# Optimization experiments

Hardware: AMD Instinct MI355X
Metric: run time of the kernel (lower is better)

Reference implementation:

```python
import jax, jax.numpy as jnp
import numpy as np
import math

M = 0.2
S = 30.0
COS_M = math.cos(M); SIN_M = math.sin(M)
TH = math.cos(math.pi - M)          # threshold used in torch.where
MM = math.sin(math.pi - M) * M      # linear penalty past threshold
EPS_LS = 0.1                        # CrossEntropyLoss label_smoothing


def _normalize(a, axis=-1):
    return a / jnp.clip(jnp.linalg.norm(a, axis=axis, keepdims=True), 1e-12)


def setup_inputs() -> dict:
    key = jax.random.key(0)
    k1, k2, k3, k4, k5 = jax.random.split(key, 5)
    B, D, C = 2048, 512, 10000
    x = jax.random.normal(k1, (B, D), dtype=jnp.float32)
    label = jax.random.randint(k2, (B,), 0, 1000)  # valid class ids, ~2 per class
    std = math.sqrt(2.0 / (C + D))  # xavier_normal gain=1
    weight = jax.random.normal(k3, (C, D), dtype=jnp.float32) * std    # self.weight (w)
    weight_m = jax.random.normal(k4, (C, D), dtype=jnp.float32) * std  # self.weight_m (wq)
    weight_n = jax.random.uniform(k5, (C, D), dtype=jnp.float32)       # self.weight_n (wk)
    return {"x": x, "label": label, "weight": weight, "weight_m": weight_m, "weight_n": weight_n}


def reference(x, label, weight, weight_m, weight_n):
    B = x.shape[0]
    C = weight.shape[0]
    xn = _normalize(x)                                   # [B, D]

    # ---- AAM (ArcFace) branch ----
    cosine = xn @ _normalize(weight).T                   # [B, C]
    sine = jnp.sqrt(jnp.clip(1.0 - cosine * cosine, 0.0, 1.0))
    phi = cosine * COS_M - sine * SIN_M
    phi = jnp.where(cosine - TH > 0, phi, cosine - MM)
    one_hot = jax.nn.one_hot(label, C, dtype=cosine.dtype)
    output = (one_hot * phi + (1.0 - one_hot) * cosine) * S
    logp = jax.nn.log_softmax(output, axis=-1)
    q_target = one_hot * (1.0 - EPS_LS) + EPS_LS / C     # label smoothing
    aam_loss = -jnp.mean(jnp.sum(q_target * logp, axis=-1))

    # ---- Control-Contrastive branch ----
    label_matrix = label[:, None] == label[None, :]      # [B, B] bool
    q = xn @ _normalize(weight_m[label]).T               # [B, B]
    k = xn @ _normalize(weight_n[label]).T               # [B, B]
    sim = q * k                                          # elementwise, [B, B]

    lm = label_matrix.astype(sim.dtype)
    ap_m = jnp.sum(sim * lm, axis=1) / jnp.sum(lm, axis=1)  # masked row means, [B]
    ap = jnp.diagonal(sim)                                   # [B]
    an = jnp.where(label_matrix, 0.0, sim)                   # [B, B]

    cos_ap = jnp.clip(ap, 0.0, 1.0)
    sin_ap = jnp.sqrt(jnp.clip(1.0 - cos_ap, 0.0, 1.0))
    cos_apm = jnp.clip(ap_m, 0.0, 1.0)
    sin_apm = jnp.sqrt(jnp.clip(1.0 - cos_apm, 0.0, 1.0))
    cos_an = jnp.clip(an, 0.0, 1.0)
    sin_an = jnp.sqrt(jnp.clip(1.0 - cos_an, 0.0, 1.0))

    phi_pm_c = cos_ap * cos_apm - sin_ap * sin_apm       # [B]
    phi_pm_s = jnp.sqrt(jnp.clip(1.0 - phi_pm_c, 0.0, 1.0))
    phi_pm = phi_pm_c * COS_M - phi_pm_s * SIN_M
    logit_neg = 1.0 - phi_pm                              # [B]

    # torch broadcasting [B,B]*[B] -> broadcast over rows (axis 0)
    phi_nm_s = sin_an * cos_apm[None, :] + cos_an * sin_apm[None, :]
    phi_nm_c = jnp.sqrt(jnp.clip(1.0 - phi_nm_s, 0.0, 1.0))
    phi_nm = phi_nm_s * COS_M - phi_nm_c * SIN_M          # [B, B]

    # ragged boolean-indexed logsumexp == masked logsumexp over whole matrix
    lse_n = jax.nn.logsumexp(jnp.where(label_matrix, -jnp.inf, phi_nm))
    lse_neg = jax.nn.logsumexp(logit_neg)
    cc_loss = jax.nn.softplus(lse_n + lse_neg)

    return aam_loss + cc_loss
```

## Files before the change

### kernel.cpp

```cpp
#include <hip/hip_runtime.h>
#include <hip/hip_bf16.h>

typedef unsigned short u16;
typedef unsigned char u8;
typedef unsigned int u32;
typedef _Float16 f16;
typedef _Float16 f16x8 __attribute__((ext_vector_type(8)));
typedef float f32x4 __attribute__((ext_vector_type(4)));
typedef unsigned int u32x4 __attribute__((ext_vector_type(4)));
typedef unsigned int u32x2 __attribute__((ext_vector_type(2)));
typedef long v2i64 __attribute__((ext_vector_type(2)));

constexpr int BATCH = 2048;
constexpr int DIM   = 512;
constexpr int NCLS  = 10000;
constexpr int NPAD  = 10240;

#define F_S     30.0f
#define F_COS_M 0.9800665778412416f
#define F_SIN_M 0.19866933079506122f
#define F_TH   (-0.9800665778412416f)
#define F_MM    0.03973386615901224f

#define G_AAM  1280
#define G_CC    512

static __device__ __forceinline__ float clampf(float v, float lo, float hi) {
    return fminf(fmaxf(v, lo), hi);
}
static __device__ __forceinline__ u32 pk4_fp8(float a, float b, float c, float d) {
    u32 w = __builtin_amdgcn_cvt_pk_fp8_f32(a, b, 0, false);
    w = __builtin_amdgcn_cvt_pk_fp8_f32(c, d, w, true);
    return w;
}
static __device__ __forceinline__ void glds16(const void* g, void* l) {
    __builtin_amdgcn_global_load_lds(
        (const __attribute__((address_space(1))) unsigned int*)g,
        (__attribute__((address_space(3))) unsigned int*)l, 16, 0, 0);
}
static __device__ __forceinline__ float blk_sum(float v, float* sh, int t) {
#pragma unroll
    for (int o = 32; o > 0; o >>= 1) v += __shfl_down(v, o, 64);
    __syncthreads();
    if ((t & 63) == 0) sh[t >> 6] = v;
    __syncthreads();
    return sh[0] + sh[1] + sh[2] + sh[3];
}

__global__ __launch_bounds__(256) void norm_all_kernel(const float* __restrict__ x,
                                                       const float* __restrict__ w,
                                                       const float* __restrict__ wm,
                                                       const float* __restrict__ wn,
                                                       const int* __restrict__ label,
                                                       u8* __restrict__ xnb,
                                                       u8* __restrict__ wb,
                                                       u8* __restrict__ wqb,
                                                       u8* __restrict__ wkb,
                                                       float* __restrict__ zacc) {
    const int t = threadIdx.x, lane = t & 63, wv = t >> 6;
    const int b = blockIdx.x;
    if (b < 33) zacc[b * 256 + t] = 0.f;

    const int row = b * 4 + wv;
    const float* src;
    u8* dst;
    if (row < BATCH) {
        src = x + (size_t)row * DIM;
        dst = xnb + (size_t)row * DIM;
    } else if (row < BATCH + NPAD) {
        const int r = row - BATCH;
        dst = wb + (size_t)r * DIM;
        if (r >= NCLS) {
            u32x2 z = {0, 0};
            *(u32x2*)(dst + lane * 8) = z;
            return;
        }
        src = w + (size_t)r * DIM;
    } else if (row < BATCH + NPAD + BATCH) {
        const int i = row - (BATCH + NPAD);
        src = wm + (size_t)label[i] * DIM;
        dst = wqb + (size_t)i * DIM;
    } else {
        const int i = row - (BATCH + NPAD + BATCH);
        src = wn + (size_t)label[i] * DIM;
        dst = wkb + (size_t)i * DIM;
    }
    const float4 v0 = ((const float4*)src)[lane * 2];
    const float4 v1 = ((const float4*)src)[lane * 2 + 1];
    float s = v0.x * v0.x + v0.y * v0.y + v0.z * v0.z + v0.w * v0.w
            + v1.x * v1.x + v1.y * v1.y + v1.z * v1.z + v1.w * v1.w;
#pragma unroll
    for (int o = 32; o > 0; o >>= 1) s += __shfl_xor(s, o, 64);
    const float inv = 1.0f / fmaxf(sqrtf(s), 1e-12f);
    u32 lo = pk4_fp8(v0.x * inv, v0.y * inv, v0.z * inv, v0.w * inv);
    u32 hi = pk4_fp8(v1.x * inv, v1.y * inv, v1.z * inv, v1.w * inv);
    const int p = 8 * (lane >> 3) + 4 * (lane & 1) + ((lane >> 1) & 3);
    u32x2 o2;
    o2[0] = __shfl(lo, p, 64);
    o2[1] = __shfl(hi, p, 64);
    *(u32x2*)(dst + lane * 8) = o2;
}

__global__ __launch_bounds__(256, 4) void gemm_fused_kernel(const u8* __restrict__ A,
                                                            const u8* __restrict__ Bw,
                                                            const u8* __restrict__ Bq,
                                                            const u8* __restrict__ Bk,
                                                            const int* __restrict__ label,
                                                            float* __restrict__ sumexp,
                                                            float* __restrict__ sumlogit,
                                                            float* __restrict__ philab,
                                                            f16* __restrict__ sim,
                                                            float* __restrict__ msum,
                                                            float* __restrict__ mcnt,
                                                            float* __restrict__ ap) {
    __shared__ __align__(16) u8 sA[2][8192];
    __shared__ __align__(16) u8 sB[2][8192];
    __shared__ float red0[128];
    __shared__ float red1[128];

    const int t = threadIdx.x;
    const int lane = t & 63, wave = t >> 6;
    const int fr = lane & 15, quad = lane >> 4;
    const int gl = quad ^ ((fr >> 1) & 3);

    if (t < 128) { red0[t] = 0.f; red1[t] = 0.f; }

    const int srow = t >> 2;
    const int sg   = (t & 3) ^ ((t >> 3) & 3);

    if (blockIdx.x < G_AAM) {
        const int flat = blockIdx.x;
        const int xcd = flat & 7, r = flat >> 3;
        const int bm = r & 15;
        const int bn = (r >> 4) * 8 + xcd;

        const int wm = (wave >> 1) * 64, wn = (wave & 1) * 64;
        const u8* ag = A  + (size_t)(bm * 128 + srow) * DIM + sg * 16;
        const u8* bg = Bw + (size_t)(bn * 128 + srow) * DIM + sg * 16;

        f32x4 acc[4][4] = {};

#define STAGE_AAM(buf, ko)                                              \
        do {                                                            \
            glds16(ag + (ko),            &sA[buf][t * 16]);             \
            glds16(ag + 64 * DIM + (ko), &sA[buf][4096 + t * 16]);      \
            glds16(bg + (ko),            &sB[buf][t * 16]);             \
            glds16(bg + 64 * DIM + (ko), &sB[buf][4096 + t * 16]);      \
        } while (0)

        STAGE_AAM(0, 0);
#pragma unroll
        for (int kb = 0; kb < 8; kb++) {
            const int cur = kb & 1;
            if (kb < 7) {
                STAGE_AAM(cur ^ 1, (kb + 1) * 64);
                asm volatile("s_waitcnt vmcnt(4)" ::: "memory");
            } else {
                asm volatile("s_waitcnt vmcnt(0)" ::: "memory");
            }
            __builtin_amdgcn_s_barrier();
            asm volatile("" ::: "memory");

            const u8* sAc = sA[cur];
            const u8* sBc = sB[cur];
            v2i64 a8[4], b8[4];
#pragma unroll
            for (int f = 0; f < 4; f++) {
                a8[f] = __builtin_bit_cast(v2i64, *(const u32x4*)&sAc[(wm + f * 16 + fr) * 64 + gl * 16]);
                b8[f] = __builtin_bit_cast(v2i64, *(const u32x4*)&sBc[(wn + f * 16 + fr) * 64 + gl * 16]);
            }
            __builtin_amdgcn_s_setprio(1);
#pragma unroll
            for (int i = 0; i < 4; i++)
#pragma unroll
                for (int j = 0; j < 4; j++) {
                    acc[i][j] = __builtin_amdgcn_mfma_f32_16x16x32_fp8_fp8(a8[i][0], b8[j][0], acc[i][j], 0, 0, 0);
                    acc[i][j] = __builtin_amdgcn_mfma_f32_16x16x32_fp8_fp8(a8[i][1], b8[j][1], acc[i][j], 0, 0, 0);
                }
            __builtin_amdgcn_s_setprio(0);
            asm volatile("s_waitcnt lgkmcnt(0)" ::: "memory");
            __builtin_amdgcn_s_barrier();
            asm volatile("" ::: "memory");
        }
#undef STAGE_AAM

#pragma unroll
        for (int i = 0; i < 4; i++) {
#pragma unroll
            for (int r3 = 0; r3 < 4; r3++) {
                const int ml = wm + i * 16 + quad * 4 + r3;
                const int mg = bm * 128 + ml;
                const int lab = label[mg];
                float esum = 0.f, lsum = 0.f;
#pragma unroll
                for (int j = 0; j < 4; j++) {
                    const int ng = bn * 128 + wn + j * 16 + fr;
                    if (ng < NCLS) {
                        float cv = acc[i][j][r3];
                        float logit;
                        if (ng == lab) {
                            float sine = sqrtf(clampf(1.f - cv * cv, 0.f, 1.f));
                            float phi = cv * F_COS_M - sine * F_SIN_M;
                            float val = ((cv - F_TH) > 0.f) ? phi : (cv - F_MM);
                            logit = F_S * val;
                            philab[mg] = logit;
                        } else {
                            logit = F_S * cv;
                        }
                        esum += __expf(logit);
                        lsum += logit;
                    }
                }
#pragma unroll
                for (int off = 1; off < 16; off <<= 1) {
                    esum += __shfl_xor(esum, off, 64);
                    lsum += __shfl_xor(lsum, off, 64);
                }
                if (fr == 0) {
                    atomicAdd(&red0[ml], esum);
                    atomicAdd(&red1[ml], lsum);
                }
            }
        }
        __syncthreads();
        if (t < 128) {
            atomicAdd(&sumexp[bm * 128 + t], red0[t]);
            atomicAdd(&sumlogit[bm * 128 + t], red1[t]);
        }
    } else {
        const int c = blockIdx.x - G_AAM;
        const int xcd = c & 7, r = c >> 3;
        const int bm = r & 15;
        const int bn = (r >> 4) * 8 + xcd;

        const int wm = (wave >> 1) * 64, wn = (wave & 1) * 32;

        const u8* ag = A  + (size_t)(bm * 128 + srow) * DIM + sg * 16;
        const u8* qg = Bq + (size_t)(bn * 64 + srow) * DIM + sg * 16;
        const u8* kg = Bk + (size_t)(bn * 64 + srow) * DIM + sg * 16;

        f32x4 aq[4][2] = {};
        f32x4 ak[4][2] = {};

#define STAGE_CC(buf, ko)                                               \
        do {                                                            \
            glds16(ag + (ko),            &sA[buf][t * 16]);             \
            glds16(ag + 64 * DIM + (ko), &sA[buf][4096 + t * 16]);      \
            glds16(qg + (ko),            &sB[buf][t * 16]);             \
            glds16(kg + (ko),            &sB[buf][4096 + t * 16]);      \
        } while (0)

        STAGE_CC(0, 0);
#pragma unroll
        for (int kb = 0; kb < 8; kb++) {
            const int cur = kb & 1;
            if (kb < 7) {
                STAGE_CC(cur ^ 1, (kb + 1) * 64);
                asm volatile("s_waitcnt vmcnt(4)" ::: "memory");
            } else {
                asm volatile("s_waitcnt vmcnt(0)" ::: "memory");
            }
            __builtin_amdgcn_s_barrier();
            asm volatile("" ::: "memory");

            const u8* sAc = sA[cur];
            const u8* sBc = sB[cur];
            v2i64 a8[4], q8[2], k8[2];
#pragma unroll
            for (int f = 0; f < 4; f++)
                a8[f] = __builtin_bit_cast(v2i64, *(const u32x4*)&sAc[(wm + f * 16 + fr) * 64 + gl * 16]);
#pragma unroll
            for (int f = 0; f < 2; f++) {
                q8[f] = __builtin_bit_cast(v2i64, *(const u32x4*)&sBc[(wn + f * 16 + fr) * 64 + gl * 16]);
                k8[f] = __builtin_bit_cast(v2i64, *(const u32x4*)&sBc[4096 + (wn + f * 16 + fr) * 64 + gl * 16]);
            }
            __builtin_amdgcn_s_setprio(1);
#pragma unroll
            for (int i = 0; i < 4; i++)
#pragma unroll
                for (int j = 0; j < 2; j++) {
                    aq[i][j] = __builtin_amdgcn_mfma_f32_16x16x32_fp8_fp8(a8[i][0], q8[j][0], aq[i][j], 0, 0, 0);
                    aq[i][j] = __builtin_amdgcn_mfma_f32_16x16x32_fp8_fp8(a8[i][1], q8[j][1], aq[i][j], 0, 0, 0);
                    ak[i][j] = __builtin_amdgcn_mfma_f32_16x16x32_fp8_fp8(a8[i][0], k8[j][0], ak[i][j], 0, 0, 0);
                    ak[i][j] = __builtin_amdgcn_mfma_f32_16x16x32_fp8_fp8(a8[i][1], k8[j][1], ak[i][j], 0, 0, 0);
                }
            __builtin_amdgcn_s_setprio(0);
            asm volatile("s_waitcnt lgkmcnt(0)" ::: "memory");
            __builtin_amdgcn_s_barrier();
            asm volatile("" ::: "memory");
        }
#undef STAGE_CC

        int lab_n[2];
#pragma unroll
        for (int j = 0; j < 2; j++) lab_n[j] = label[bn * 64 + wn + j * 16 + fr];

#pragma unroll
        for (int i = 0; i < 4; i++) {
#pragma unroll
            for (int r3 = 0; r3 < 4; r3++) {
                const int ml = wm + i * 16 + quad * 4 + r3;
                const int mg = bm * 128 + ml;
                const int lm = label[mg];
                float ms = 0.f, mc = 0.f;
#pragma unroll
                for (int j = 0; j < 2; j++) {
                    const int ng = bn * 64 + wn + j * 16 + fr;
                    float s = aq[i][j][r3] * ak[i][j][r3];
                    sim[(size_t)mg * BATCH + ng] = (f16)s;
                    if (lab_n[j] == lm) { ms += s; mc += 1.f; }
                    if (mg == ng) ap[mg] = s;
                }
#pragma unroll
                for (int off = 1; off < 16; off <<= 1) {
                    ms += __shfl_xor(ms, off, 64);
                    mc += __shfl_xor(mc, off, 64);
                }
                if (fr == 0) {
                    atomicAdd(&red0[ml], ms);
                    atomicAdd(&red1[ml], mc);
                }
            }
        }
        __syncthreads();
        if (t < 128) {
            atomicAdd(&msum[bm * 128 + t], red0[t]);
            atomicAdd(&mcnt[bm * 128 + t], red1[t]);
        }
    }
}

__global__ __launch_bounds__(256) void cc_pass2_kernel(const f16* __restrict__ sim,
                                                       const int* __restrict__ label,
                                                       const float* __restrict__ msum,
                                                       const float* __restrict__ mcnt,
                                                       const float* __restrict__ ap,
                                                       const float* __restrict__ sumexp,
                                                       const float* __restrict__ sumlogit,
                                                       const float* __restrict__ philab,
                                                       float* __restrict__ znP,
                                                       float* __restrict__ znegP,
                                                       float* __restrict__ accAP,
                                                       unsigned* __restrict__ tick,
                                                       float* __restrict__ out) {
    __shared__ float sh[4];
    const int t = threadIdx.x, b = blockIdx.x;
    const int r0 = b * 8;

    const int4 l0 = ((const int4*)label)[t * 2];
    const int4 l1 = ((const int4*)label)[t * 2 + 1];
    const f32x4 ms0 = ((const f32x4*)msum)[t * 2];
    const f32x4 ms1 = ((const f32x4*)msum)[t * 2 + 1];
    const f32x4 mc0 = ((const f32x4*)mcnt)[t * 2];
    const f32x4 mc1 = ((const f32x4*)mcnt)[t * 2 + 1];

    f16x8 v[8];
#pragma unroll
    for (int r = 0; r < 8; r++)
        v[r] = ((const f16x8*)(sim + (size_t)(r0 + r) * BATCH))[t];

    int lj[8];
    float caj[8], saj[8];
#pragma unroll
    for (int e = 0; e < 8; e++) {
        lj[e] = (e < 4) ? ((const int*)&l0)[e] : ((const int*)&l1)[e - 4];
        const float msj = (e < 4) ? ms0[e] : ms1[e - 4];
        const float mcj = (e < 4) ? mc0[e] : mc1[e - 4];
        caj[e] = clampf(msj / mcj, 0.f, 1.f);
        saj[e] = sqrtf(clampf(1.f - caj[e], 0.f, 1.f));
    }

    float acc = 0.f;
#pragma unroll
    for (int r = 0; r < 8; r++) {
        const int li = label[r0 + r];
#pragma unroll
        for (int e = 0; e < 8; e++) {
            if (lj[e] != li) {
                float can = clampf((float)v[r][e], 0.f, 1.f);
                float san = sqrtf(clampf(1.f - can, 0.f, 1.f));
                float pns = san * caj[e] + can * saj[e];
                float pnc = sqrtf(clampf(1.f - pns, 0.f, 1.f));
                acc += __expf(pns * F_COS_M - pnc * F_SIN_M);
            }
        }
    }
    acc = blk_sum(acc, sh, t);

    const int bk = b & 31;
    if (t < 8) {
        const int rr = r0 + t;
        float lse = logf(sumexp[rr]);
        float apart = 0.9f * (philab[rr] - lse) + 1e-5f * (sumlogit[rr] - (float)NCLS * lse);
        float cam = clampf(msum[rr] / mcnt[rr], 0.f, 1.f);
        float sam = sqrtf(clampf(1.f - cam, 0.f, 1.f));
        float cap = clampf(ap[rr], 0.f, 1.f);
        float sap = sqrtf(clampf(1.f - cap, 0.f, 1.f));
        float ppc = cap * cam - sap * sam;
        float pps = sqrtf(clampf(1.f - ppc, 0.f, 1.f));
        float epart = __expf(1.f - (ppc * F_COS_M - pps * F_SIN_M));

        if (t == 0) atomicAdd(&znP[bk], acc);
        atomicAdd(&accAP[bk], apart);
        atomicAdd(&znegP[bk], epart);
    }
    if (t == 0) {
        asm volatile("s_waitcnt vmcnt(0)" ::: "memory");
        unsigned old = __hip_atomic_fetch_add(tick, 1u, __ATOMIC_RELAXED, __HIP_MEMORY_SCOPE_AGENT);
        if (old == 255u) {
            float znv = 0.f, aav = 0.f, zgv = 0.f;
            for (int k = 0; k < 32; k++) {
                znv += __hip_atomic_load(znP + k,   __ATOMIC_RELAXED, __HIP_MEMORY_SCOPE_AGENT);
                aav += __hip_atomic_load(accAP + k, __ATOMIC_RELAXED, __HIP_MEMORY_SCOPE_AGENT);
                zgv += __hip_atomic_load(znegP + k, __ATOMIC_RELAXED, __HIP_MEMORY_SCOPE_AGENT);
            }
            float aam = -aav / (float)BATCH;
            float z = logf(znv) + logf(zgv);
            float cc = (z > 0.f) ? (z + log1pf(__expf(-z))) : log1pf(__expf(z));
            out[0] = aam + cc;
        }
    }
}

extern "C" void kernel_launch(void* const* d_in, const int* in_sizes, int n_in,
                              void* d_out, int out_size, void* d_ws, size_t ws_size,
                              hipStream_t stream) {
    const float* x        = (const float*)d_in[0];
    const int*   label    = (const int*)d_in[1];
    const float* weight   = (const float*)d_in[2];
    const float* weight_m = (const float*)d_in[3];
    const float* weight_n = (const float*)d_in[4];
    float* out = (float*)d_out;
    char* ws = (char*)d_ws;

    const size_t o_xnb  = 0;
    const size_t o_wb   = o_xnb + (size_t)BATCH * DIM;
    const size_t o_wqb  = o_wb  + (size_t)NPAD * DIM;
    const size_t o_wkb  = o_wqb + (size_t)BATCH * DIM;
    const size_t o_sim  = o_wkb + (size_t)BATCH * DIM;
    const size_t o_misc = o_sim + (size_t)BATCH * BATCH * 2;

    u8* xnb = (u8*)(ws + o_xnb);
    u8* wb  = (u8*)(ws + o_wb);
    u8* wqb = (u8*)(ws + o_wqb);
    u8* wkb = (u8*)(ws + o_wkb);
    f16* sim = (f16*)(ws + o_sim);
    float* mf  = (float*)(ws + o_misc);

    float* sumexp   = mf;
    float* sumlogit = mf + 2048;
    float* msum     = mf + 4096;
    float* mcnt     = mf + 6144;
    float* znP      = mf + 8192;
    float* znegP    = mf + 8224;
    float* accAP    = mf + 8256;
    unsigned* tick  = (unsigned*)(mf + 8288);
    float* philab  = mf + 8448;
    float* ap      = mf + 10496;

    norm_all_kernel<<<(BATCH + NPAD + 2 * BATCH) / 4, 256, 0, stream>>>(
        x, weight, weight_m, weight_n, label, xnb, wb, wqb, wkb, mf);

    gemm_fused_kernel<<<G_AAM + G_CC, 256, 0, stream>>>(
        xnb, wb, wqb, wkb, label,
        sumexp, sumlogit, philab, sim, msum, mcnt, ap);

    cc_pass2_kernel<<<256, 256, 0, stream>>>(
        sim, label, msum, mcnt, ap,
        sumexp, sumlogit, philab, znP, znegP, accAP, tick, out);
}
```

Baseline: 153.7 us.

## Repartition cc_pass2 into 512 blocks of 1024 threads with 4 rows each

The second contrastive pass now launches 512 blocks of 1024 threads. Each thread handles 2 columns across 4 rows, instead of 256 blocks of 256 threads each handling 8 columns across 8 rows. The block reduction changes to 16 waves, and the completion ticket threshold becomes 511. The aim is more parallelism and latency hiding for the exp/sqrt-heavy masked logsumexp on the B×B similarity matrix. The cost is narrower 4-byte loads per row, more blocks, and more atomics on the partial accumulators.

```diff
diff --git a/kernel.cpp b/kernel.cpp
--- a/kernel.cpp
+++ b/kernel.cpp
@@ -5,6 +5,7 @@
 typedef unsigned char u8;
 typedef unsigned int u32;
 typedef _Float16 f16;
+typedef _Float16 f16x2 __attribute__((ext_vector_type(2)));
 typedef _Float16 f16x8 __attribute__((ext_vector_type(8)));
 typedef float f32x4 __attribute__((ext_vector_type(4)));
 typedef unsigned int u32x4 __attribute__((ext_vector_type(4)));
@@ -37,14 +38,6 @@
     __builtin_amdgcn_global_load_lds(
         (const __attribute__((address_space(1))) unsigned int*)g,
         (__attribute__((address_space(3))) unsigned int*)l, 16, 0, 0);
-}
-static __device__ __forceinline__ float blk_sum(float v, float* sh, int t) {
-#pragma unroll
-    for (int o = 32; o > 0; o >>= 1) v += __shfl_down(v, o, 64);
-    __syncthreads();
-    if ((t & 63) == 0) sh[t >> 6] = v;
-    __syncthreads();
-    return sh[0] + sh[1] + sh[2] + sh[3];
 }
 
 __global__ __launch_bounds__(256) void norm_all_kernel(const float* __restrict__ x,
@@ -330,52 +323,49 @@
     }
 }
 
-__global__ __launch_bounds__(256) void cc_pass2_kernel(const f16* __restrict__ sim,
-                                                       const int* __restrict__ label,
-                                                       const float* __restrict__ msum,
-                                                       const float* __restrict__ mcnt,
-                                                       const float* __restrict__ ap,
-                                                       const float* __restrict__ sumexp,
-                                                       const float* __restrict__ sumlogit,
-                                                       const float* __restrict__ philab,
-                                                       float* __restrict__ znP,
-                                                       float* __restrict__ znegP,
-                                                       float* __restrict__ accAP,
-                                                       unsigned* __restrict__ tick,
-                                                       float* __restrict__ out) {
-    __shared__ float sh[4];
+__global__ __launch_bounds__(1024) void cc_pass2_kernel(const f16* __restrict__ sim,
+                                                        const int* __restrict__ label,
+                                                        const float* __restrict__ msum,
+                                                        const float* __restrict__ mcnt,
+                                                        const float* __restrict__ ap,
+                                                        const float* __restrict__ sumexp,
+                                                        const float* __restrict__ sumlogit,
+                                                        const float* __restrict__ philab,
+                                                        float* __restrict__ znP,
+                                                        float* __restrict__ znegP,
+                                                        float* __restrict__ accAP,
+                                                        unsigned* __restrict__ tick,
+                                                        float* __restrict__ out) {
+    __shared__ float sh[16];
     const int t = threadIdx.x, b = blockIdx.x;
-    const int r0 = b * 8;
-
-    const int4 l0 = ((const int4*)label)[t * 2];
-    const int4 l1 = ((const int4*)label)[t * 2 + 1];
-    const f32x4 ms0 = ((const f32x4*)msum)[t * 2];
-    const f32x4 ms1 = ((const f32x4*)msum)[t * 2 + 1];
-    const f32x4 mc0 = ((const f32x4*)mcnt)[t * 2];
-    const f32x4 mc1 = ((const f32x4*)mcnt)[t * 2 + 1];
-
-    f16x8 v[8];
-#pragma unroll
-    for (int r = 0; r < 8; r++)
-        v[r] = ((const f16x8*)(sim + (size_t)(r0 + r) * BATCH))[t];
-
-    int lj[8];
-    float caj[8], saj[8];
-#pragma unroll
-    for (int e = 0; e < 8; e++) {
-        lj[e] = (e < 4) ? ((const int*)&l0)[e] : ((const int*)&l1)[e - 4];
-        const float msj = (e < 4) ? ms0[e] : ms1[e - 4];
-        const float mcj = (e < 4) ? mc0[e] : mc1[e - 4];
-        caj[e] = clampf(msj / mcj, 0.f, 1.f);
-        saj[e] = sqrtf(clampf(1.f - caj[e], 0.f, 1.f));
+    const int lane = t & 63, wave = t >> 6;
+    const int r0 = b * 4;
+
+    const int2   lp  = ((const int2*)label)[t];
+    const float2 msp = ((const float2*)msum)[t];
+    const float2 mcp = ((const float2*)mcnt)[t];
+
+    f16x2 v[4];
+#pragma unroll
+    for (int r = 0; r < 4; r++)
+        v[r] = ((const f16x2*)(sim + (size_t)(r0 + r) * BATCH))[t];
+
+    int lj[2];
+    float caj[2], saj[2];
+    lj[0] = lp.x; lj[1] = lp.y;
+    {
+        float c0 = clampf(msp.x / mcp.x, 0.f, 1.f);
+        float c1 = clampf(msp.y / mcp.y, 0.f, 1.f);
+        caj[0] = c0; saj[0] = sqrtf(clampf(1.f - c0, 0.f, 1.f));
+        caj[1] = c1; saj[1] = sqrtf(clampf(1.f - c1, 0.f, 1.f));
     }
 
     float acc = 0.f;
 #pragma unroll
-    for (int r = 0; r < 8; r++) {
+    for (int r = 0; r < 4; r++) {
         const int li = label[r0 + r];
 #pragma unroll
-        for (int e = 0; e < 8; e++) {
+        for (int e = 0; e < 2; e++) {
             if (lj[e] != li) {
                 float can = clampf((float)v[r][e], 0.f, 1.f);
                 float san = sqrtf(clampf(1.f - can, 0.f, 1.f));
@@ -385,10 +375,13 @@
             }
         }
     }
-    acc = blk_sum(acc, sh, t);
+#pragma unroll
+    for (int o = 32; o > 0; o >>= 1) acc += __shfl_down(acc, o, 64);
+    if (lane == 0) sh[wave] = acc;
+    __syncthreads();
 
     const int bk = b & 31;
-    if (t < 8) {
+    if (t < 4) {
         const int rr = r0 + t;
         float lse = logf(sumexp[rr]);
         float apart = 0.9f * (philab[rr] - lse) + 1e-5f * (sumlogit[rr] - (float)NCLS * lse);
@@ -400,14 +393,19 @@
         float pps = sqrtf(clampf(1.f - ppc, 0.f, 1.f));
         float epart = __expf(1.f - (ppc * F_COS_M - pps * F_SIN_M));
 
-        if (t == 0) atomicAdd(&znP[bk], acc);
+        if (t == 0) {
+            float asum = 0.f;
+#pragma unroll
+            for (int k = 0; k < 16; k++) asum += sh[k];
+            atomicAdd(&znP[bk], asum);
+        }
         atomicAdd(&accAP[bk], apart);
         atomicAdd(&znegP[bk], epart);
     }
     if (t == 0) {
         asm volatile("s_waitcnt vmcnt(0)" ::: "memory");
         unsigned old = __hip_atomic_fetch_add(tick, 1u, __ATOMIC_RELAXED, __HIP_MEMORY_SCOPE_AGENT);
-        if (old == 255u) {
+        if (old == 511u) {
             float znv = 0.f, aav = 0.f, zgv = 0.f;
             for (int k = 0; k < 32; k++) {
                 znv += __hip_atomic_load(znP + k,   __ATOMIC_RELAXED, __HIP_MEMORY_SCOPE_AGENT);
@@ -465,7 +463,7 @@
         xnb, wb, wqb, wkb, label,
         sumexp, sumlogit, philab, sim, msum, mcnt, ap);
 
-    cc_pass2_kernel<<<256, 256, 0, stream>>>(
+    cc_pass2_kernel<<<512, 1024, 0, stream>>>(
         sim, label, msum, mcnt, ap,
         sumexp, sumlogit, philab, znP, znegP, accAP, tick, out);
 }
```

Measured after the change: 156.4 us. No clear change (+1.8%).
